# Performance work log

Hardware: AMD Instinct MI355X
Metric: run time of the kernel (lower is better)

The kernel has to match this reference:

```python
import jax, jax.numpy as jnp
import numpy as np

N_NODES = 50000
N_EDGES = 800000
IN_DIM = 256
OUT_DIM = 768
D_SCALE = OUT_DIM // 3  # 256, must equal IN_DIM so repeated conv application type-checks
SCALES = [1, 2, 4]


def setup_inputs() -> dict:
    key = jax.random.key(0)
    ks = jax.random.split(key, 12)
    x = jax.random.normal(ks[0], (N_NODES, IN_DIM), dtype=jnp.float32)
    edge_index = jax.random.randint(ks[1], (2, N_EDGES), 0, N_NODES, dtype=jnp.int64)
    edge_attr = jax.random.uniform(ks[2], (N_EDGES, 1), dtype=jnp.float32)
    s = 1.0 / np.sqrt(IN_DIM)
    W1 = jax.random.uniform(ks[3], (IN_DIM, D_SCALE), jnp.float32, -s, s)
    b1 = jnp.zeros((D_SCALE,), jnp.float32)
    W2 = jax.random.uniform(ks[4], (IN_DIM, D_SCALE), jnp.float32, -s, s)
    b2 = jnp.zeros((D_SCALE,), jnp.float32)
    W3 = jax.random.uniform(ks[5], (IN_DIM, D_SCALE), jnp.float32, -s, s)
    b3 = jnp.zeros((D_SCALE,), jnp.float32)
    sp = 1.0 / np.sqrt(OUT_DIM)
    Wp = jax.random.uniform(ks[6], (OUT_DIM, OUT_DIM), jnp.float32, -sp, sp)
    bp = jax.random.uniform(ks[7], (OUT_DIM,), jnp.float32, -sp, sp)
    gamma = jnp.ones((OUT_DIM,), jnp.float32)
    beta = jnp.zeros((OUT_DIM,), jnp.float32)
    return {"x": x, "edge_index": edge_index, "edge_attr": edge_attr,
            "W1": W1, "b1": b1, "W2": W2, "b2": b2, "W3": W3, "b3": b3,
            "Wp": Wp, "bp": bp, "gamma": gamma, "beta": beta}


def _gcn_conv(x, src, dst, norm, W, b):
    # PyG GCNConv: h = x @ W; out[i] = sum_{(j->i)} norm_e * h[j]; + bias
    h = x @ W                                   # [N, D]
    msg = h[src] * norm[:, None]                # [E+N, D] edge gather (memory-bound)
    out = jax.ops.segment_sum(msg, dst, num_segments=N_NODES)
    return out + b


def reference(x, edge_index, edge_attr, W1, b1, W2, b2, W3, b3, Wp, bp, gamma, beta):
    ew = edge_attr.squeeze(-1)
    src = edge_index[0]
    dst = edge_index[1]
    # add self-loops with weight 1 (GCNConv default, fill_value=1)
    loop = jnp.arange(N_NODES, dtype=src.dtype)
    src_a = jnp.concatenate([src, loop])
    dst_a = jnp.concatenate([dst, loop])
    w_a = jnp.concatenate([ew, jnp.ones((N_NODES,), ew.dtype)])
    deg = jax.ops.segment_sum(w_a, dst_a, num_segments=N_NODES)
    dinv = jnp.where(deg > 0, jax.lax.rsqrt(deg), 0.0)
    norm = dinv[src_a] * w_a * dinv[dst_a]      # symmetric normalization per edge

    feats = []
    for (W, b), scale in zip([(W1, b1), (W2, b2), (W3, b3)], SCALES):
        f = x
        for _ in range(scale):
            f = _gcn_conv(f, src_a, dst_a, norm, W, b)
        feats.append(f)
    out = jnp.concatenate(feats, axis=1)        # [N, OUT_DIM]
    out = out @ Wp + bp
    mu = jnp.mean(out, axis=-1, keepdims=True)
    var = jnp.var(out, axis=-1, keepdims=True)
    out = (out - mu) * jax.lax.rsqrt(var + 1e-5) * gamma + beta
    return jax.nn.gelu(out, approximate=False)
```

## Files before the change

### kernel.cpp

```cpp
#include <hip/hip_runtime.h>
#include <math.h>

#define NN 50000
#define NE 800000
#define DIN 256
#define DOUT 768
#define NPAD 50176
#define NBS 196

typedef _Float16 half8 __attribute__((ext_vector_type(8)));
typedef _Float16 half4 __attribute__((ext_vector_type(4)));
typedef float    f32x4 __attribute__((ext_vector_type(4)));

__global__ void init_deg_cnt(float* __restrict__ deg, int* __restrict__ cnt) {
    int i = blockIdx.x * 256 + threadIdx.x;
    if (i < NN) { deg[i] = 1.0f; cnt[i] = 0; }
}

__global__ void edge_deg_cnt(const int* __restrict__ ei, const float* __restrict__ ea,
                             float* __restrict__ deg, int* __restrict__ cnt) {
    int e = blockIdx.x * 256 + threadIdx.x;
    if (e >= NE) return;
    int dst = ei[NE + e];
    atomicAdd(&deg[dst], ea[e]);
    atomicAdd(&cnt[dst], 1);
}

__global__ void compute_dinv(const float* __restrict__ deg, float* __restrict__ dinv) {
    int i = blockIdx.x * 256 + threadIdx.x;
    if (i < NN) { float d = deg[i]; dinv[i] = d > 0.f ? rsqrtf(d) : 0.f; }
}

__global__ __launch_bounds__(256) void scan_bsum(const int* __restrict__ cnt,
                                                 int* __restrict__ bsum) {
    int i = blockIdx.x * 256 + threadIdx.x;
    int v = (i < NN) ? cnt[i] : 0;
#pragma unroll
    for (int m = 1; m < 64; m <<= 1) v += __shfl_xor(v, m);
    __shared__ int ws[4];
    int wave = threadIdx.x >> 6, lane = threadIdx.x & 63;
    if (lane == 0) ws[wave] = v;
    __syncthreads();
    if (threadIdx.x == 0) bsum[blockIdx.x] = ws[0] + ws[1] + ws[2] + ws[3];
}

__global__ __launch_bounds__(256) void scan_boff(const int* __restrict__ bsum,
                                                 int* __restrict__ boff) {
    int t = threadIdx.x;
    int v = (t < NBS) ? bsum[t] : 0;
    int lane = t & 63, wave = t >> 6, orig = v;
#pragma unroll
    for (int d = 1; d < 64; d <<= 1) {
        int u = __shfl_up(v, d);
        if (lane >= d) v += u;
    }
    __shared__ int ws[4];
    if (lane == 63) ws[wave] = v;
    __syncthreads();
    int wp = 0;
#pragma unroll
    for (int w2 = 0; w2 < 4; ++w2) if (w2 < wave) wp += ws[w2];
    if (t < NBS) boff[t] = wp + v - orig;
}

__global__ __launch_bounds__(256) void scan_write(const int* __restrict__ cnt,
                                                  const int* __restrict__ boff,
                                                  int* __restrict__ rowp,
                                                  int* __restrict__ cursor) {
    int b = blockIdx.x, t = threadIdx.x;
    int i = b * 256 + t;
    int v = (i < NN) ? cnt[i] : 0;
    int lane = t & 63, wave = t >> 6, orig = v;
#pragma unroll
    for (int d = 1; d < 64; d <<= 1) {
        int u = __shfl_up(v, d);
        if (lane >= d) v += u;
    }
    __shared__ int ws[4];
    if (lane == 63) ws[wave] = v;
    __syncthreads();
    int wp = 0;
#pragma unroll
    for (int w2 = 0; w2 < 4; ++w2) if (w2 < wave) wp += ws[w2];
    int excl = boff[b] + wp + v - orig;
    if (i < NN) { rowp[i] = excl; cursor[i] = excl; }
    if (i == NN - 1) rowp[NN] = NE;
}

__global__ void edge_scatter(const int* __restrict__ ei, const float* __restrict__ ea,
                             const float* __restrict__ dinv, int* __restrict__ cursor,
                             int* __restrict__ col, float* __restrict__ val) {
    int e = blockIdx.x * 256 + threadIdx.x;
    if (e >= NE) return;
    int s = ei[e];
    int d = ei[NE + e];
    int pos = atomicAdd(&cursor[d], 1);
    col[pos] = s;
    val[pos] = dinv[s] * ea[e] * dinv[d];
}

__global__ void x2h_kernel(const float* __restrict__ x, _Float16* __restrict__ Xh) {
    int i = blockIdx.x * 256 + threadIdx.x;
    if (i >= NN * DIN / 4) return;
    float4 v = ((const float4*)x)[i];
    half4 h; h[0] = (_Float16)v.x; h[1] = (_Float16)v.y;
    h[2] = (_Float16)v.z; h[3] = (_Float16)v.w;
    ((half4*)Xh)[i] = h;
}

__device__ inline float rv(const float* __restrict__ R, int c) {
    return R ? R[c] : 1.f;
}

__global__ __launch_bounds__(256) void agg_kernel(
        const _Float16* __restrict__ Gin, int sIn,
        _Float16* __restrict__ Gout, int sOut,
        const float* __restrict__ Rin, float* __restrict__ Rout,
        const int* __restrict__ rowp, const int* __restrict__ colv,
        const float* __restrict__ val, const float* __restrict__ dinv) {
    int node = blockIdx.x * 4 + (threadIdx.x >> 6);
    if (node >= NN) return;
    int lane = threadIdx.x & 63;
    const _Float16* gb = Gin + lane * 4;
    float acc[4] = {0.f, 0.f, 0.f, 0.f};
    float racc = 0.f;
    int beg = rowp[node], end = rowp[node + 1];
    int k = beg;
    for (; k + 8 <= end; k += 8) {
        int   c0 = colv[k+0], c1 = colv[k+1], c2 = colv[k+2], c3 = colv[k+3];
        int   c4 = colv[k+4], c5 = colv[k+5], c6 = colv[k+6], c7 = colv[k+7];
        float v0 = val[k+0], v1 = val[k+1], v2 = val[k+2], v3 = val[k+3];
        float v4 = val[k+4], v5 = val[k+5], v6 = val[k+6], v7 = val[k+7];
        half4 g0 = *(const half4*)(gb + (size_t)c0 * sIn);
        half4 g1 = *(const half4*)(gb + (size_t)c1 * sIn);
        half4 g2 = *(const half4*)(gb + (size_t)c2 * sIn);
        half4 g3 = *(const half4*)(gb + (size_t)c3 * sIn);
        half4 g4 = *(const half4*)(gb + (size_t)c4 * sIn);
        half4 g5 = *(const half4*)(gb + (size_t)c5 * sIn);
        half4 g6 = *(const half4*)(gb + (size_t)c6 * sIn);
        half4 g7 = *(const half4*)(gb + (size_t)c7 * sIn);
#pragma unroll
        for (int j = 0; j < 4; ++j)
            acc[j] += v0 * (float)g0[j] + v1 * (float)g1[j]
                    + v2 * (float)g2[j] + v3 * (float)g3[j]
                    + v4 * (float)g4[j] + v5 * (float)g5[j]
                    + v6 * (float)g6[j] + v7 * (float)g7[j];
        if (Rout)
            racc += v0 * rv(Rin, c0) + v1 * rv(Rin, c1)
                  + v2 * rv(Rin, c2) + v3 * rv(Rin, c3)
                  + v4 * rv(Rin, c4) + v5 * rv(Rin, c5)
                  + v6 * rv(Rin, c6) + v7 * rv(Rin, c7);
    }
    for (; k + 4 <= end; k += 4) {
        int   c0 = colv[k+0], c1 = colv[k+1], c2 = colv[k+2], c3 = colv[k+3];
        float v0 = val[k+0], v1 = val[k+1], v2 = val[k+2], v3 = val[k+3];
        half4 g0 = *(const half4*)(gb + (size_t)c0 * sIn);
        half4 g1 = *(const half4*)(gb + (size_t)c1 * sIn);
        half4 g2 = *(const half4*)(gb + (size_t)c2 * sIn);
        half4 g3 = *(const half4*)(gb + (size_t)c3 * sIn);
#pragma unroll
        for (int j = 0; j < 4; ++j)
            acc[j] += v0 * (float)g0[j] + v1 * (float)g1[j]
                    + v2 * (float)g2[j] + v3 * (float)g3[j];
        if (Rout)
            racc += v0 * rv(Rin, c0) + v1 * rv(Rin, c1)
                  + v2 * rv(Rin, c2) + v3 * rv(Rin, c3);
    }
    for (; k < end; ++k) {
        int c = colv[k]; float v = val[k];
        half4 g = *(const half4*)(gb + (size_t)c * sIn);
#pragma unroll
        for (int j = 0; j < 4; ++j) acc[j] += v * (float)g[j];
        if (Rout) racc += v * rv(Rin, c);
    }
    float dv = dinv[node], sv = dv * dv;
    half4 gs = *(const half4*)(gb + (size_t)node * sIn);
#pragma unroll
    for (int j = 0; j < 4; ++j) acc[j] += sv * (float)gs[j];
    half4 o;
#pragma unroll
    for (int j = 0; j < 4; ++j) o[j] = (_Float16)acc[j];
    *(half4*)(Gout + (size_t)node * sOut + lane * 4) = o;
    if (Rout && lane == 0)
        Rout[node] = racc + sv * (Rin ? Rin[node] : 1.f);
}

__global__ __launch_bounds__(256) void wp1(
        const float* __restrict__ W2, const float* __restrict__ W3,
        const float* __restrict__ b2, const float* __restrict__ b3,
        float* __restrict__ W2sq, float* __restrict__ W3_2,
        float* __restrict__ bw2, float* __restrict__ bw3a) {
    int b = blockIdx.x, j = threadIdx.x;
    const float* A; const float* B; float* C;
    if (b < 256)      { A = W2 + b * 256;         B = W2; C = W2sq + b * 256; }
    else if (b < 512) { A = W3 + (b - 256) * 256; B = W3; C = W3_2 + (b - 256) * 256; }
    else if (b == 512){ A = b2;                   B = W2; C = bw2; }
    else              { A = b3;                   B = W3; C = bw3a; }
    float s = 0.f;
#pragma unroll 8
    for (int k = 0; k < 256; ++k) s += A[k] * B[k * 256 + j];
    C[j] = s;
}

__global__ __launch_bounds__(256) void wp2(
        const float* __restrict__ W3_2, const float* __restrict__ W3,
        const float* __restrict__ bw3a,
        float* __restrict__ W3_4, float* __restrict__ bw3b) {
    int b = blockIdx.x, j = threadIdx.x;
    const float* A; const float* B; float* C;
    if (b < 256) { A = W3_2 + b * 256; B = W3_2; C = W3_4 + b * 256; }
    else         { A = bw3a;           B = W3;   C = bw3b; }
    float s = 0.f;
#pragma unroll 8
    for (int k = 0; k < 256; ++k) s += A[k] * B[k * 256 + j];
    C[j] = s;
}

__global__ __launch_bounds__(256) void wp3(
        const float* __restrict__ W1, const float* __restrict__ W2sq,
        const float* __restrict__ W3_4, const float* __restrict__ Wp,
        const float* __restrict__ W3, const float* __restrict__ bw3b,
        _Float16* __restrict__ Mt, float* __restrict__ bw3c) {
    int b = blockIdx.x, j = threadIdx.x;
    if (b == 768) {
        float s = 0.f;
#pragma unroll 8
        for (int k = 0; k < 256; ++k) s += bw3b[k] * W3[k * 256 + j];
        bw3c[j] = s;
        return;
    }
    int kk = b;
    int blk = kk >> 8;
    const float* A = (blk == 0) ? (W1 + kk * 256)
                   : (blk == 1) ? (W2sq + (kk - 256) * 256)
                                : (W3_4 + (kk - 512) * 256);
    const float* B = Wp + (size_t)(blk * 256) * 768;
    float s0 = 0.f, s1 = 0.f, s2 = 0.f;
#pragma unroll 4
    for (int m = 0; m < 256; ++m) {
        float a = A[m];
        const float* br = B + (size_t)m * 768;
        s0 += a * br[j]; s1 += a * br[j + 256]; s2 += a * br[j + 512];
    }
    Mt[(size_t)j * 768 + kk]         = (_Float16)s0;
    Mt[(size_t)(j + 256) * 768 + kk] = (_Float16)s1;
    Mt[(size_t)(j + 512) * 768 + kk] = (_Float16)s2;
}

__global__ __launch_bounds__(256) void wp4(
        const float* __restrict__ Wp,
        const float* __restrict__ b1, const float* __restrict__ b2,
        const float* __restrict__ b3, const float* __restrict__ bp,
        const float* __restrict__ bw2, const float* __restrict__ bw3a,
        const float* __restrict__ bw3b, const float* __restrict__ bw3c,
        float* __restrict__ u1, float* __restrict__ u2,
        float* __restrict__ u3, float* __restrict__ c0) {
    int vec = blockIdx.x / 3, chunk = blockIdx.x % 3;
    int j = chunk * 256 + threadIdx.x;
    const float* P1 = Wp;
    const float* P2 = Wp + (size_t)256 * 768;
    const float* P3 = Wp + (size_t)512 * 768;
    float s = 0.f;
    if (vec == 0) {
#pragma unroll 8
        for (int k = 0; k < 256; ++k) s += bw2[k] * P2[(size_t)k * 768 + j];
#pragma unroll 8
        for (int k = 0; k < 256; ++k) s += bw3a[k] * P3[(size_t)k * 768 + j];
        u1[j] = s;
    } else if (vec == 1) {
#pragma unroll 8
        for (int k = 0; k < 256; ++k) s += bw3b[k] * P3[(size_t)k * 768 + j];
        u2[j] = s;
    } else if (vec == 2) {
#pragma unroll 8
        for (int k = 0; k < 256; ++k) s += bw3c[k] * P3[(size_t)k * 768 + j];
        u3[j] = s;
    } else {
#pragma unroll 8
        for (int k = 0; k < 256; ++k) s += b1[k] * P1[(size_t)k * 768 + j];
#pragma unroll 8
        for (int k = 0; k < 256; ++k) s += b2[k] * P2[(size_t)k * 768 + j];
#pragma unroll 8
        for (int k = 0; k < 256; ++k) s += b3[k] * P3[(size_t)k * 768 + j];
        c0[j] = s + bp[j];
    }
}

__device__ inline void g2lds16(const void* g, void* l) {
    __builtin_amdgcn_global_load_lds(
        (__attribute__((address_space(1))) void*)g,
        (__attribute__((address_space(3))) void*)l, 16, 0, 0);
}

__global__ __launch_bounds__(256) void gemm_mfma(
        const _Float16* __restrict__ A,
        const _Float16* __restrict__ Bt,
        float* __restrict__ C, int M,
        const float* __restrict__ R1, const float* __restrict__ R2,
        const float* __restrict__ R3,
        const float* __restrict__ u1, const float* __restrict__ u2,
        const float* __restrict__ u3, const float* __restrict__ c0) {
    __shared__ _Float16 As[2][128 * 64];
    __shared__ _Float16 Bs[2][128 * 64];
    const int tid  = threadIdx.x;
    const int wid  = tid >> 6;
    const int lane = tid & 63;
    const int lid  = blockIdx.y * (DOUT / 128) + blockIdx.x;
    const int pair = (lid & 7) * (NPAD / 128 * (DOUT / 128) / 8) + (lid >> 3);
    const int bm = (pair / (DOUT / 128)) * 128;
    const int bn = (pair % (DOUT / 128)) * 128;
    const int wm = (wid >> 1) * 64;
    const int wn = (wid & 1) * 64;
    const int l15  = lane & 15;
    const int quad = lane >> 4;

    f32x4 acc[4][4] = {};

    auto stage = [&](int buf, int k0) {
#pragma unroll
        for (int it = 0; it < 4; ++it) {
            int row = wid * 32 + it * 8 + (lane >> 3);
            int lc  = ((lane & 7) - row) & 7;
            const _Float16* ga = A  + (size_t)(bm + row) * DOUT + k0 + lc * 8;
            const _Float16* gb = Bt + (size_t)(bn + row) * DOUT + k0 + lc * 8;
            g2lds16(ga, &As[buf][(size_t)(wid * 32 + it * 8) * 64]);
            g2lds16(gb, &Bs[buf][(size_t)(wid * 32 + it * 8) * 64]);
        }
    };

    const int NT = DOUT / 64;
    stage(0, 0);
    __syncthreads();
    int cur = 0;
    for (int t = 0; t < NT; ++t) {
        if (t + 1 < NT) stage(cur ^ 1, (t + 1) * 64);
        half8 af[2][4], bf[2][4];
#pragma unroll
        for (int i = 0; i < 4; ++i) {
            int ra = wm + i * 16 + l15;
            int rb = wn + i * 16 + l15;
#pragma unroll
            for (int h = 0; h < 2; ++h) {
                int pa = ((h * 4 + quad) + ra) & 7;
                af[h][i] = *(const half8*)(&As[cur][(size_t)ra * 64 + pa * 8]);
                int pb = ((h * 4 + quad) + rb) & 7;
                bf[h][i] = *(const half8*)(&Bs[cur][(size_t)rb * 64 + pb * 8]);
            }
        }
#pragma unroll
        for (int mi = 0; mi < 4; ++mi)
#pragma unroll
            for (int ni = 0; ni < 4; ++ni) {
                acc[mi][ni] = __builtin_amdgcn_mfma_f32_16x16x32_f16(
                    af[0][mi], bf[0][ni], acc[mi][ni], 0, 0, 0);
                acc[mi][ni] = __builtin_amdgcn_mfma_f32_16x16x32_f16(
                    af[1][mi], bf[1][ni], acc[mi][ni], 0, 0, 0);
            }
        __syncthreads();
        cur ^= 1;
    }

    float e0[4], e1[4], e2[4], e3[4];
#pragma unroll
    for (int ni = 0; ni < 4; ++ni) {
        int gc = bn + wn + ni * 16 + l15;
        e0[ni] = c0[gc]; e1[ni] = u1[gc]; e2[ni] = u2[gc]; e3[ni] = u3[gc];
    }
#pragma unroll
    for (int mi = 0; mi < 4; ++mi) {
#pragma unroll
        for (int r = 0; r < 4; ++r) {
            int gr = bm + wm + mi * 16 + quad * 4 + r;
            if (gr >= M) continue;
            float r1 = R1[gr], r2 = R2[gr], r3 = R3[gr];
#pragma unroll
            for (int ni = 0; ni < 4; ++ni) {
                int gc = bn + wn + ni * 16 + l15;
                C[(size_t)gr * DOUT + gc] =
                    acc[mi][ni][r] + e0[ni] + r1 * e1[ni] + r2 * e2[ni] + r3 * e3[ni];
            }
        }
    }
}

__global__ __launch_bounds__(256) void ln_gelu_kernel(float* __restrict__ out,
        const float* __restrict__ gamma, const float* __restrict__ beta) {
    int row = blockIdx.x;
    int t = threadIdx.x;
    float* p = out + (size_t)row * DOUT;
    float x0 = p[t], x1 = p[t + 256], x2 = p[t + 512];
    float s = x0 + x1 + x2;
    float s2 = x0 * x0 + x1 * x1 + x2 * x2;
    __shared__ float red[8];
    int wave = t >> 6, lane = t & 63;
#pragma unroll
    for (int m = 1; m < 64; m <<= 1) {
        s += __shfl_xor(s, m);
        s2 += __shfl_xor(s2, m);
    }
    if (lane == 0) { red[wave] = s; red[4 + wave] = s2; }
    __syncthreads();
    float S = red[0] + red[1] + red[2] + red[3];
    float S2 = red[4] + red[5] + red[6] + red[7];
    float mu = S * (1.f / 768.f);
    float var = S2 * (1.f / 768.f) - mu * mu;
    float inv = rsqrtf(var + 1e-5f);
    const float kk = 0.70710678118654752f;
#pragma unroll
    for (int i = 0; i < 3; ++i) {
        int c = t + 256 * i;
        float x = (i == 0) ? x0 : (i == 1) ? x1 : x2;
        float y = (x - mu) * inv * gamma[c] + beta[c];
        p[c] = 0.5f * y * (1.f + erff(y * kk));
    }
}

extern "C" void kernel_launch(void* const* d_in, const int* in_sizes, int n_in,
                              void* d_out, int out_size, void* d_ws, size_t ws_size,
                              hipStream_t stream) {
    const float* x     = (const float*)d_in[0];
    const int*   ei    = (const int*)d_in[1];
    const float* ea    = (const float*)d_in[2];
    const float* W1    = (const float*)d_in[3];
    const float* b1    = (const float*)d_in[4];
    const float* W2    = (const float*)d_in[5];
    const float* b2    = (const float*)d_in[6];
    const float* W3    = (const float*)d_in[7];
    const float* b3    = (const float*)d_in[8];
    const float* Wp    = (const float*)d_in[9];
    const float* bp    = (const float*)d_in[10];
    const float* gamma = (const float*)d_in[11];
    const float* beta  = (const float*)d_in[12];
    float* out = (float*)d_out;

    char* w = (char*)d_ws;
    auto alloc = [&](size_t bytes) -> void* {
        void* p = (void*)w;
        w += (bytes + 255) & ~(size_t)255;
        return p;
    };
    _Float16* Acat = (_Float16*)alloc((size_t)NPAD * DOUT * 2);
    _Float16* Xh   = (_Float16*)alloc((size_t)NN * DIN * 2);
    _Float16* G3h  = (_Float16*)alloc((size_t)NN * DIN * 2);
    _Float16* Mt   = (_Float16*)alloc((size_t)DOUT * DOUT * 2);
    int*   col    = (int*)alloc((size_t)NE * 4);
    float* val    = (float*)alloc((size_t)NE * 4);
    float* deg    = (float*)alloc((size_t)NN * 4);
    float* dinv   = (float*)alloc((size_t)NN * 4);
    int*   cnt    = (int*)alloc((size_t)NN * 4);
    int*   rowp   = (int*)alloc((size_t)(NN + 1) * 4);
    int*   cursor = (int*)alloc((size_t)NN * 4);
    int*   bsum   = (int*)alloc((size_t)NBS * 4);
    int*   boff   = (int*)alloc((size_t)NBS * 4);
    float* R1     = (float*)alloc((size_t)NN * 4);
    float* R2     = (float*)alloc((size_t)NN * 4);
    float* R3     = (float*)alloc((size_t)NN * 4);
    float* W2sq   = (float*)alloc(256 * 256 * 4);
    float* W3_2   = (float*)alloc(256 * 256 * 4);
    float* W3_4   = (float*)alloc(256 * 256 * 4);
    float* bw2    = (float*)alloc(256 * 4);
    float* bw3a   = (float*)alloc(256 * 4);
    float* bw3b   = (float*)alloc(256 * 4);
    float* bw3c   = (float*)alloc(256 * 4);
    float* u1     = (float*)alloc(768 * 4);
    float* u2     = (float*)alloc(768 * 4);
    float* u3     = (float*)alloc(768 * 4);
    float* c0     = (float*)alloc(768 * 4);

    const int nb_n = (NN + 255) / 256;
    const int nb_e = (NE + 255) / 256;

    init_deg_cnt<<<nb_n, 256, 0, stream>>>(deg, cnt);
    edge_deg_cnt<<<nb_e, 256, 0, stream>>>(ei, ea, deg, cnt);
    compute_dinv<<<nb_n, 256, 0, stream>>>(deg, dinv);
    scan_bsum<<<NBS, 256, 0, stream>>>(cnt, bsum);
    scan_boff<<<1, 256, 0, stream>>>(bsum, boff);
    scan_write<<<NBS, 256, 0, stream>>>(cnt, boff, rowp, cursor);
    edge_scatter<<<nb_e, 256, 0, stream>>>(ei, ea, dinv, cursor, col, val);

    x2h_kernel<<<(NN * DIN / 4 + 255) / 256, 256, 0, stream>>>(x, Xh);

    wp1<<<514, 256, 0, stream>>>(W2, W3, b2, b3, W2sq, W3_2, bw2, bw3a);
    wp2<<<257, 256, 0, stream>>>(W3_2, W3, bw3a, W3_4, bw3b);
    wp3<<<769, 256, 0, stream>>>(W1, W2sq, W3_4, Wp, W3, bw3b, Mt, bw3c);
    wp4<<<12, 256, 0, stream>>>(Wp, b1, b2, b3, bp, bw2, bw3a, bw3b, bw3c,
                                u1, u2, u3, c0);

    const int nb_a = (NN + 3) / 4;
    agg_kernel<<<nb_a, 256, 0, stream>>>(Xh, DIN,          Acat + 0,   DOUT, nullptr, R1, rowp, col, val, dinv);
    agg_kernel<<<nb_a, 256, 0, stream>>>(Acat + 0,   DOUT, Acat + 256, DOUT, R1,      R2, rowp, col, val, dinv);
    agg_kernel<<<nb_a, 256, 0, stream>>>(Acat + 256, DOUT, G3h,        DIN,  R2,      R3, rowp, col, val, dinv);
    agg_kernel<<<nb_a, 256, 0, stream>>>(G3h,        DIN,  Acat + 512, DOUT, nullptr, nullptr, rowp, col, val, dinv);

    dim3 grid(DOUT / 128, NPAD / 128);
    gemm_mfma<<<grid, 256, 0, stream>>>(Acat, Mt, out, NN, R1, R2, R3, u1, u2, u3, c0);

    ln_gelu_kernel<<<NN, 256, 0, stream>>>(out, gamma, beta);
}
```

Baseline: 860.8 us.

## Store GEMM output in fp16, use wave-per-row LayerNorm, and refine GEMM pipeline sync

The GEMM now writes its pre-LayerNorm result as fp16 into a workspace buffer instead of fp32 into the output, which halves both the GEMM store traffic and the LayerNorm read traffic. The LayerNorm+GELU kernel now handles one row per wave with vectorized loads and a shuffle-only reduction, dropping the shared-memory reduction and block barrier. The GEMM main loop swaps __syncthreads for explicit vmcnt waits, s_barrier and sched_barriers so the next tile's loads can overlap compute. Rounding pre-norm values to fp16 before LayerNorm lowers precision.

```diff
diff --git a/kernel.cpp b/kernel.cpp
--- a/kernel.cpp
+++ b/kernel.cpp
@@ -295,7 +295,7 @@
 __global__ __launch_bounds__(256) void gemm_mfma(
         const _Float16* __restrict__ A,
         const _Float16* __restrict__ Bt,
-        float* __restrict__ C, int M,
+        _Float16* __restrict__ Ch, int M,
         const float* __restrict__ R1, const float* __restrict__ R2,
         const float* __restrict__ R3,
         const float* __restrict__ u1, const float* __restrict__ u2,
@@ -330,10 +330,17 @@
 
     const int NT = DOUT / 64;
     stage(0, 0);
-    __syncthreads();
     int cur = 0;
     for (int t = 0; t < NT; ++t) {
-        if (t + 1 < NT) stage(cur ^ 1, (t + 1) * 64);
+        if (t + 1 < NT) {
+            stage(cur ^ 1, (t + 1) * 64);
+            __builtin_amdgcn_sched_barrier(0);
+            asm volatile("s_waitcnt vmcnt(8)" ::: "memory");
+        } else {
+            asm volatile("s_waitcnt vmcnt(0)" ::: "memory");
+        }
+        __builtin_amdgcn_s_barrier();
+        __builtin_amdgcn_sched_barrier(0);
         half8 af[2][4], bf[2][4];
 #pragma unroll
         for (int i = 0; i < 4; ++i) {
@@ -356,7 +363,8 @@
                 acc[mi][ni] = __builtin_amdgcn_mfma_f32_16x16x32_f16(
                     af[1][mi], bf[1][ni], acc[mi][ni], 0, 0, 0);
             }
-        __syncthreads();
+        __builtin_amdgcn_sched_barrier(0);
+        __builtin_amdgcn_s_barrier();
         cur ^= 1;
     }
 
@@ -376,42 +384,58 @@
 #pragma unroll
             for (int ni = 0; ni < 4; ++ni) {
                 int gc = bn + wn + ni * 16 + l15;
-                C[(size_t)gr * DOUT + gc] =
-                    acc[mi][ni][r] + e0[ni] + r1 * e1[ni] + r2 * e2[ni] + r3 * e3[ni];
+                Ch[(size_t)gr * DOUT + gc] = (_Float16)(
+                    acc[mi][ni][r] + e0[ni] + r1 * e1[ni] + r2 * e2[ni] + r3 * e3[ni]);
             }
         }
     }
 }
 
-__global__ __launch_bounds__(256) void ln_gelu_kernel(float* __restrict__ out,
+__global__ __launch_bounds__(256) void ln_gelu_kernel(
+        const _Float16* __restrict__ Ch, float* __restrict__ out,
         const float* __restrict__ gamma, const float* __restrict__ beta) {
-    int row = blockIdx.x;
-    int t = threadIdx.x;
-    float* p = out + (size_t)row * DOUT;
-    float x0 = p[t], x1 = p[t + 256], x2 = p[t + 512];
-    float s = x0 + x1 + x2;
-    float s2 = x0 * x0 + x1 * x1 + x2 * x2;
-    __shared__ float red[8];
-    int wave = t >> 6, lane = t & 63;
+    int row = blockIdx.x * 4 + (threadIdx.x >> 6);
+    if (row >= NN) return;
+    int lane = threadIdx.x & 63;
+    const _Float16* p = Ch + (size_t)row * DOUT;
+    half4 h0 = *(const half4*)(p + lane * 4);
+    half4 h1 = *(const half4*)(p + 256 + lane * 4);
+    half4 h2 = *(const half4*)(p + 512 + lane * 4);
+    float v[12];
+#pragma unroll
+    for (int j = 0; j < 4; ++j) {
+        v[j]     = (float)h0[j];
+        v[4 + j] = (float)h1[j];
+        v[8 + j] = (float)h2[j];
+    }
+    float s = 0.f, s2 = 0.f;
+#pragma unroll
+    for (int j = 0; j < 12; ++j) { s += v[j]; s2 += v[j] * v[j]; }
 #pragma unroll
     for (int m = 1; m < 64; m <<= 1) {
         s += __shfl_xor(s, m);
         s2 += __shfl_xor(s2, m);
     }
-    if (lane == 0) { red[wave] = s; red[4 + wave] = s2; }
-    __syncthreads();
-    float S = red[0] + red[1] + red[2] + red[3];
-    float S2 = red[4] + red[5] + red[6] + red[7];
-    float mu = S * (1.f / 768.f);
-    float var = S2 * (1.f / 768.f) - mu * mu;
+    float mu = s * (1.f / 768.f);
+    float var = s2 * (1.f / 768.f) - mu * mu;
     float inv = rsqrtf(var + 1e-5f);
     const float kk = 0.70710678118654752f;
+    float* po = out + (size_t)row * DOUT;
 #pragma unroll
     for (int i = 0; i < 3; ++i) {
-        int c = t + 256 * i;
-        float x = (i == 0) ? x0 : (i == 1) ? x1 : x2;
-        float y = (x - mu) * inv * gamma[c] + beta[c];
-        p[c] = 0.5f * y * (1.f + erff(y * kk));
+        int c = i * 256 + lane * 4;
+        float4 g = *(const float4*)(gamma + c);
+        float4 b = *(const float4*)(beta + c);
+        float4 o;
+        float y0 = (v[i * 4 + 0] - mu) * inv * g.x + b.x;
+        float y1 = (v[i * 4 + 1] - mu) * inv * g.y + b.y;
+        float y2 = (v[i * 4 + 2] - mu) * inv * g.z + b.z;
+        float y3 = (v[i * 4 + 3] - mu) * inv * g.w + b.w;
+        o.x = 0.5f * y0 * (1.f + erff(y0 * kk));
+        o.y = 0.5f * y1 * (1.f + erff(y1 * kk));
+        o.z = 0.5f * y2 * (1.f + erff(y2 * kk));
+        o.w = 0.5f * y3 * (1.f + erff(y3 * kk));
+        *(float4*)(po + c) = o;
     }
 }
 
@@ -442,6 +466,7 @@
     _Float16* Acat = (_Float16*)alloc((size_t)NPAD * DOUT * 2);
     _Float16* Xh   = (_Float16*)alloc((size_t)NN * DIN * 2);
     _Float16* G3h  = (_Float16*)alloc((size_t)NN * DIN * 2);
+    _Float16* Ch   = (_Float16*)alloc((size_t)NN * DOUT * 2);
     _Float16* Mt   = (_Float16*)alloc((size_t)DOUT * DOUT * 2);
     int*   col    = (int*)alloc((size_t)NE * 4);
     float* val    = (float*)alloc((size_t)NE * 4);
@@ -493,7 +518,7 @@
     agg_kernel<<<nb_a, 256, 0, stream>>>(G3h,        DIN,  Acat + 512, DOUT, nullptr, nullptr, rowp, col, val, dinv);
 
     dim3 grid(DOUT / 128, NPAD / 128);
-    gemm_mfma<<<grid, 256, 0, stream>>>(Acat, Mt, out, NN, R1, R2, R3, u1, u2, u3, c0);
-
-    ln_gelu_kernel<<<NN, 256, 0, stream>>>(out, gamma, beta);
-}
+    gemm_mfma<<<grid, 256, 0, stream>>>(Acat, Mt, Ch, NN, R1, R2, R3, u1, u2, u3, c0);
+
+    ln_gelu_kernel<<<(NN + 3) / 4, 256, 0, stream>>>(Ch, out, gamma, beta);
+}
```

Measured after the change: 815.8 us. 1.06x faster.
